# Performance work log

Measured on AMD Instinct MI355X. Metric: run time of the kernel, lower is better.

## Reference

```python
import jax, jax.numpy as jnp
import numpy as np

B, L, DIN = 2048, 70, 15
HID, NF, K = 16, 4, 40          # hidden_units//2, n_features, kernel_size
C = DIN + 1 + NF                # 20 signature input channels (original + time + conv features)
Z0 = 64
SIG_CH = C + C * C + C ** 3     # 8420, depth-3 signature channels


def setup_inputs() -> dict:
    key = jax.random.key(0)
    ks = jax.random.split(key, 8)
    return {
        "observed_data": jax.random.normal(ks[0], (B, L, DIN), jnp.float32),
        "observed_tp": jnp.linspace(0.0, 1.0, L, dtype=jnp.float32),
        "conv1_w": jax.random.normal(ks[1], (HID, DIN, K), jnp.float32) / np.float32(np.sqrt(DIN * K)),
        "conv1_b": jnp.zeros((HID,), jnp.float32),
        "conv2_w": jax.random.normal(ks[2], (HID, HID), jnp.float32) / np.float32(np.sqrt(HID)),
        "conv2_b": jnp.zeros((HID,), jnp.float32),
        "conv3_w": jax.random.normal(ks[3], (NF, HID), jnp.float32) / np.float32(np.sqrt(HID)),
        "conv3_b": jnp.zeros((NF,), jnp.float32),
        "w_out": jax.random.normal(ks[4], (2 * Z0, SIG_CH), jnp.float32) * np.float32(np.sqrt(2.0 / (SIG_CH + 2 * Z0))),
        "b_out": jnp.zeros((2 * Z0,), jnp.float32),
    }


def _augment(x, w1, b1, w2, b2, w3, b3):
    # x: (B, L, DIN).  signatory.Augment: conv(K) -> relu -> conv1x1 -> relu -> conv1x1,
    # then concat [truncated original, time channel, conv features] along channels.
    xc = jnp.transpose(x, (0, 2, 1))                                   # (B, DIN, L)
    h = jax.lax.conv_general_dilated(xc, w1, (1,), 'VALID')            # (B, HID, Lp)
    h = h + b1[None, :, None]
    h = jnp.einsum('oc,bcl->bol', w2, jax.nn.relu(h)) + b2[None, :, None]
    h = jnp.einsum('oc,bcl->bol', w3, jax.nn.relu(h)) + b3[None, :, None]
    conv_out = jnp.transpose(h, (0, 2, 1))                             # (B, Lp, NF)
    Lp = conv_out.shape[1]
    orig = x[:, K - 1:, :]                                             # (B, Lp, DIN)
    t = jnp.linspace(0.0, 1.0, Lp, dtype=x.dtype)
    time = jnp.broadcast_to(t[None, :, None], (x.shape[0], Lp, 1))
    return jnp.concatenate([orig, time, conv_out], axis=2)             # (B, Lp, C)


def _signature_depth3(path):
    # Truncated (depth 3) path signature with basepoint=True, via Chen's identity:
    # S <- S \otimes exp(dx) over increments, zero basepoint prepended.
    incs = jnp.diff(path, axis=1, prepend=jnp.zeros_like(path[:, :1]))  # (B, Lp, C)
    incs = jnp.transpose(incs, (1, 0, 2))                               # (Lp, B, C)
    Bn, Cn = path.shape[0], path.shape[2]
    s1 = jnp.zeros((Bn, Cn), path.dtype)
    s2 = jnp.zeros((Bn, Cn, Cn), path.dtype)
    s3 = jnp.zeros((Bn, Cn, Cn, Cn), path.dtype)

    def step(carry, d):
        s1, s2, s3 = carry
        e2 = 0.5 * d[:, :, None] * d[:, None, :]                        # d\otimes d / 2
        e3 = (e2[:, :, :, None] * d[:, None, None, :]) / 3.0            # d^{\otimes 3} / 6
        n3 = (s3
              + s2[:, :, :, None] * d[:, None, None, :]
              + s1[:, :, None, None] * e2[:, None, :, :]
              + e3)
        n2 = s2 + s1[:, :, None] * d[:, None, :] + e2
        n1 = s1 + d
        return (n1, n2, n3), None

    (s1, s2, s3), _ = jax.lax.scan(step, (s1, s2, s3), incs)
    return jnp.concatenate([s1, s2.reshape(Bn, -1), s3.reshape(Bn, -1)], axis=1)


def reference(observed_data, observed_tp, conv1_w, conv1_b, conv2_w, conv2_b,
              conv3_w, conv3_b, w_out, b_out):
    # encode_obs_time=False -> observed_tp unused
    path = _augment(observed_data, conv1_w, conv1_b, conv2_w, conv2_b, conv3_w, conv3_b)
    sig = _signature_depth3(path)                                       # (B, SIG_CH)
    z = sig @ w_out.T + b_out                                           # (B, 2*Z0)
    mean_z0 = z[:, :Z0][None]                                           # (1, B, Z0)
    std_z0 = jax.nn.softplus(z[:, Z0:][None])                           # (1, B, Z0)
    return mean_z0, std_z0
```

## Files before the change

kernel.cpp:

```cpp
#include <hip/hip_runtime.h>
#include <math.h>

#define B_TOT 2048
#define D_INC 15
#define KW    40
#define CCH   20
#define LP    31
#define SIGCH 8420
#define SIGP  8448
#define NOUT  128
#define KSPLIT 11
#define KLEN  768

typedef _Float16 f16;
typedef _Float16 f16x8 __attribute__((ext_vector_type(8)));
typedef _Float16 f16x4 __attribute__((ext_vector_type(4)));
typedef float    f32x4 __attribute__((ext_vector_type(4)));
typedef float    f32x2 __attribute__((ext_vector_type(2)));

__global__ __launch_bounds__(256) void k_prep(const float* __restrict__ w1,
                                              f16* __restrict__ wA)
{
    const int ln = threadIdx.x & 63;
    const int wv = threadIdx.x >> 6;
    const int h  = ln & 15;
    const int q4 = ln >> 4;
    for (int gi = 0; gi < 5; ++gi) {
        int g = wv * 5 + gi;
        f16x8 v;
#pragma unroll
        for (int j = 0; j < 8; ++j) {
            int kq = q4 * 8 + j;
            int kk = 2 * g + (kq >> 4);
            int c  = kq & 15;
            v[j] = (c < D_INC) ? (f16)w1[h * 600 + c * 40 + kk] : (f16)0.f;
        }
        *(f16x8*)(wA + g * 512 + ln * 8) = v;
    }
}

__global__ __launch_bounds__(256, 2) void k_augsig(
    const float* __restrict__ x,  const f16* __restrict__ wA, const float* __restrict__ b1,
    const float* __restrict__ w2, const float* __restrict__ b2,
    const float* __restrict__ w3, const float* __restrict__ b3,
    const float* __restrict__ w_out, f16* __restrict__ wh, f16* __restrict__ sig)
{
    if (blockIdx.x >= 512) {
        int t0 = (blockIdx.x - 512) * 256 + threadIdx.x;
        for (int chunk = t0; chunk < 128 * 1056; chunk += 8192) {
            int o  = chunk / 1056;
            int cw = chunk - o * 1056;
            int c0 = cw * 8;
            f16x8 v;
            if (c0 + 8 <= SIGCH) {
                const float* src = w_out + (size_t)o * SIGCH + c0;
                float4 a = *(const float4*)src;
                float4 b = *(const float4*)(src + 4);
                v = (f16x8){(f16)a.x,(f16)a.y,(f16)a.z,(f16)a.w,
                            (f16)b.x,(f16)b.y,(f16)b.z,(f16)b.w};
            } else {
#pragma unroll
                for (int e = 0; e < 8; ++e) {
                    int c = c0 + e;
                    v[e] = (c < SIGCH) ? (f16)w_out[(size_t)o * SIGCH + c] : (f16)0.f;
                }
            }
            *(f16x8*)(wh + (size_t)o * SIGP + c0) = v;
        }
        return;
    }

    __shared__ float xs[4 * 1068];
    __shared__ f16   xp16[4 * 1152];
    __shared__ float pprev[4 * 656];
    __shared__ float wsmall[356];
    float* w2s = wsmall;        float* b2s = wsmall + 256;
    float* w3s = wsmall + 272;  float* b3s = wsmall + 336;
    float* b1s = wsmall + 340;
    float* h1s  = (float*)xp16;
    float* incs = xs;

    const int tid = threadIdx.x;
    const int b0  = blockIdx.x * 4;

    for (int i = tid; i < 4 * 1050; i += 256) {
        int bl = i / 1050; int t = i - bl * 1050;
        xs[bl * 1068 + t] = x[(size_t)b0 * 1050 + i];
    }
    if (tid < 256) w2s[tid] = w2[tid];
    if (tid < 16)  b2s[tid] = b2[tid];
    if (tid < 64)  w3s[tid] = w3[tid];
    if (tid < 4)   b3s[tid] = b3[tid];
    if (tid < 16)  b1s[tid] = b1[tid];
    __syncthreads();

    for (int r = tid; r < 280; r += 256) {
        int bl = r / 70; int pos = r - bl * 70;
        const float* src = xs + bl * 1068 + pos * 15;
        f16* dst = xp16 + bl * 1152 + pos * 16;
#pragma unroll
        for (int c = 0; c < 15; ++c) dst[c] = (f16)src[c];
        dst[15] = (f16)0.f;
    }
    __syncthreads();

    const int lane = tid & 63;
    const int w    = tid >> 6;
    const int n16  = lane & 15;
    const int q4   = lane >> 4;

    f16x8 wa[20];
#pragma unroll
    for (int g = 0; g < 20; ++g) wa[g] = *(const f16x8*)(wA + g * 512 + lane * 8);

    f32x4 cacc[2];
#pragma unroll
    for (int tile = 0; tile < 2; ++tile) {
        const int pos0 = tile * 15;
        f32x4 acc = {0.f, 0.f, 0.f, 0.f};
#pragma unroll
        for (int g = 0; g < 20; ++g) {
            const f16x8 bf = *(const f16x8*)&xp16[w * 1152 +
                (pos0 + n16 + 2 * g + (q4 >> 1)) * 16 + (q4 & 1) * 8];
            acc = __builtin_amdgcn_mfma_f32_16x16x32_f16(wa[g], bf, acc, 0, 0, 0);
        }
        cacc[tile] = acc;
    }
    __syncthreads();

#pragma unroll
    for (int tile = 0; tile < 2; ++tile) {
        int pos = tile * 15 + n16;
#pragma unroll
        for (int r = 0; r < 4; ++r) {
            int h = q4 * 4 + r;
            h1s[(w * 31 + pos) * 17 + h] = fmaxf(cacc[tile][r] + b1s[h], 0.f);
        }
    }
    __syncthreads();

    if (tid < 124) {
        const int bl2 = tid / 31;
        const int pos = tid - bl2 * 31;
        float hr[16];
#pragma unroll
        for (int c2 = 0; c2 < 16; ++c2) hr[c2] = h1s[tid * 17 + c2];
        float h2[16];
#pragma unroll
        for (int o = 0; o < 16; ++o) {
            float s = b2s[o];
#pragma unroll
            for (int c2 = 0; c2 < 16; ++c2) s += w2s[o * 16 + c2] * hr[c2];
            h2[o] = fmaxf(s, 0.f);
        }
        float h3[4];
#pragma unroll
        for (int f = 0; f < 4; ++f) {
            float s = b3s[f];
#pragma unroll
            for (int c2 = 0; c2 < 16; ++c2) s += w3s[f * 16 + c2] * h2[c2];
            h3[f] = s;
        }
        float* pr = pprev + bl2 * 656 + 20 + pos * 20;
#pragma unroll
        for (int d = 0; d < D_INC; ++d) pr[d] = xs[bl2 * 1068 + (pos + 39) * 15 + d];
        pr[15] = (float)pos * (1.0f / 30.0f);
#pragma unroll
        for (int f = 0; f < 4; ++f) pr[16 + f] = h3[f];
    } else {
        int z = tid - 124;
        if (z < 80) pprev[(z / 20) * 656 + (z % 20)] = 0.f;
    }
    __syncthreads();

    float* pp = pprev + w * 656;
    float* ic = incs  + w * 624;
    for (int i = lane; i < 620; i += 64) ic[i] = pp[20 + i] - pp[i];
    __syncthreads();

    int iv[7], jv[7];
#pragma unroll
    for (int q = 0; q < 7; ++q) {
        int p = lane + 64 * q;
        iv[q] = p / 20; jv[q] = p - iv[q] * 20;
    }
    float s2r[7];
    f32x2 s3v[7][10];
#pragma unroll
    for (int q = 0; q < 7; ++q) {
        s2r[q] = 0.f;
#pragma unroll
        for (int k = 0; k < 10; ++k) s3v[q][k] = (f32x2){0.f, 0.f};
    }

    for (int t = 0; t < LP; ++t) {
        const float* ip = &ic[t * 20];
        const float* sp = &pp[t * 20];
        f32x2 dv[10];
        const float4* dp = (const float4*)ip;
#pragma unroll
        for (int r = 0; r < 5; ++r) {
            float4 v = dp[r];
            dv[2*r]   = (f32x2){v.x, v.y};
            dv[2*r+1] = (f32x2){v.z, v.w};
        }
#pragma unroll
        for (int q = 0; q < 7; ++q) {
            if (lane + 64 * q < 400) {
                const float di  = ip[iv[q]];
                const float dj  = ip[jv[q]];
                const float s1i = sp[iv[q]];
                const float t2  = s2r[q] + (0.5f * s1i + (1.0f / 6.0f) * di) * dj;
                const f32x2 t2v = {t2, t2};
#pragma unroll
                for (int k = 0; k < 10; ++k) s3v[q][k] += t2v * dv[k];
                s2r[q] += (s1i + 0.5f * di) * dj;
            }
        }
    }

    const int b = b0 + w;
    f16* sg = sig + (size_t)b * SIGP;
    if (lane < 20) sg[lane] = (f16)pp[620 + lane];
#pragma unroll
    for (int q = 0; q < 6; ++q) sg[20 + q * 64 + lane] = (f16)s2r[q];
    if (lane < 16) sg[404 + lane] = (f16)s2r[6];
#pragma unroll
    for (int q = 0; q < 7; ++q) {
        int p = lane + 64 * q;
        if (p < 400) {
            f16* base = sg + 420 + p * 20;
#pragma unroll
            for (int g = 0; g < 5; ++g) {
                f16x4 v = { (f16)s3v[q][2*g][0],   (f16)s3v[q][2*g][1],
                            (f16)s3v[q][2*g+1][0], (f16)s3v[q][2*g+1][1] };
                *(f16x4*)(base + 4 * g) = v;
            }
        }
    }
    if (lane < 28) sg[SIGCH + lane] = (f16)0.f;
}

__global__ __launch_bounds__(256) void k_gemm(const f16* __restrict__ sigh,
                                              const f16* __restrict__ wh,
                                              float* __restrict__ z_part)
{
    __shared__ f16 As[2048];
    __shared__ f16 Bs[8192];
    const int tid = threadIdx.x;
    const int l   = tid & 63;
    const int wv  = tid >> 6;
    const int mt  = blockIdx.x / KSPLIT;
    const int s   = blockIdx.x - mt * KSPLIT;
    const int m0  = mt * 32;
    const int kb  = s * KLEN;

    const f32x4 z4 = {0.f, 0.f, 0.f, 0.f};
    f32x4 acc[2][2];
    acc[0][0] = z4; acc[0][1] = z4; acc[1][0] = z4; acc[1][1] = z4;

    const size_t gA = (size_t)(m0 + (tid & 31)) * SIGP + kb + (tid >> 5) * 8;
    size_t gB[4];
#pragma unroll
    for (int r = 0; r < 4; ++r) {
        int slot = r * 256 + tid;
        gB[r] = (size_t)(slot & 127) * SIGP + kb + (slot >> 7) * 8;
    }

    f16x8 aR = *(const f16x8*)(sigh + gA);
    f16x8 bR[4];
#pragma unroll
    for (int r = 0; r < 4; ++r) bR[r] = *(const f16x8*)(wh + gB[r]);

    const int kg   = l >> 4;
    const int mrow = l & 15;

    for (int ch = 0; ch < 12; ++ch) {
        *(f16x8*)&As[tid * 8] = aR;
#pragma unroll
        for (int r = 0; r < 4; ++r) *(f16x8*)&Bs[(r * 256 + tid) * 8] = bR[r];
        __syncthreads();

        if (ch < 11) {
            int koff = (ch + 1) * 64;
            aR = *(const f16x8*)(sigh + gA + koff);
#pragma unroll
            for (int r = 0; r < 4; ++r) bR[r] = *(const f16x8*)(wh + gB[r] + koff);
        }

#pragma unroll
        for (int kc = 0; kc < 2; ++kc) {
            f16x8 aF[2], bF[2];
#pragma unroll
            for (int m2 = 0; m2 < 2; ++m2)
                aF[m2] = *(const f16x8*)&As[((kc * 4 + kg) * 32 + m2 * 16 + mrow) * 8];
#pragma unroll
            for (int n2 = 0; n2 < 2; ++n2)
                bF[n2] = *(const f16x8*)&Bs[((kc * 4 + kg) * 128 + wv * 32 + n2 * 16 + mrow) * 8];
#pragma unroll
            for (int m2 = 0; m2 < 2; ++m2)
#pragma unroll
                for (int n2 = 0; n2 < 2; ++n2)
                    acc[m2][n2] = __builtin_amdgcn_mfma_f32_16x16x32_f16(aF[m2], bF[n2], acc[m2][n2], 0, 0, 0);
        }
        __syncthreads();
    }

#pragma unroll
    for (int m2 = 0; m2 < 2; ++m2) {
#pragma unroll
        for (int n2 = 0; n2 < 2; ++n2) {
            int n = wv * 32 + n2 * 16 + (l & 15);
#pragma unroll
            for (int r = 0; r < 4; ++r) {
                int m = m0 + m2 * 16 + (l >> 4) * 4 + r;
                z_part[((size_t)s * B_TOT + m) * NOUT + n] = acc[m2][n2][r];
            }
        }
    }
}

__global__ __launch_bounds__(256) void k_final(const float* __restrict__ z_part,
                                               const float* __restrict__ b_out,
                                               float* __restrict__ out)
{
    int idx = blockIdx.x * 256 + threadIdx.x;
    int b = idx >> 7;
    int o = idx & 127;
    float z = b_out[o];
#pragma unroll
    for (int s = 0; s < KSPLIT; ++s) z += z_part[((size_t)s * B_TOT + b) * NOUT + o];
    if (o < 64) {
        out[(size_t)b * 64 + o] = z;
    } else {
        float sp = fmaxf(z, 0.f) + log1pf(expf(-fabsf(z)));
        out[131072 + (size_t)b * 64 + (o - 64)] = sp;
    }
}

extern "C" void kernel_launch(void* const* d_in, const int* in_sizes, int n_in,
                              void* d_out, int out_size, void* d_ws, size_t ws_size,
                              hipStream_t stream)
{
    const float* x     = (const float*)d_in[0];
    const float* w1    = (const float*)d_in[2];
    const float* b1    = (const float*)d_in[3];
    const float* w2    = (const float*)d_in[4];
    const float* b2    = (const float*)d_in[5];
    const float* w3    = (const float*)d_in[6];
    const float* b3    = (const float*)d_in[7];
    const float* w_out = (const float*)d_in[8];
    const float* b_out = (const float*)d_in[9];
    float* out = (float*)d_out;

    float* ws    = (float*)d_ws;
    f16*   sigh  = (f16*)ws;
    f16*   wh    = (f16*)(ws + 8650752);
    f16*   wA    = (f16*)(ws + 9191424);
    float* zpart = ws + 9196544;

    hipLaunchKernelGGL(k_prep,   dim3(1),    dim3(256), 0, stream, w1, wA);
    hipLaunchKernelGGL(k_augsig, dim3(544),  dim3(256), 0, stream,
                       x, wA, b1, w2, b2, w3, b3, w_out, wh, sigh);
    hipLaunchKernelGGL(k_gemm,   dim3(704),  dim3(256), 0, stream, sigh, wh, zpart);
    hipLaunchKernelGGL(k_final,  dim3(1024), dim3(256), 0, stream, zpart, b_out, out);
}
```

Measured before the change: 154.0 us.

## Compute depth-3 signature via MFMA over time with suffix-sum formulation

Replaces the per-lane sequential Chen-identity scan, which held 140 fp32 accumulators per lane, with a closed-form sum over time steps. Level-3 terms become products of per-step factors (a_i*d_j, e_i*d_j) contracted against a matrix of suffix sums of increments. Level 2 comes from a ones column. The contraction runs on 16x16x32 f16 MFMA. Shared memory is merged into one pool so per-warp buffers can reuse the input staging area. The change cuts register pressure and VALU work, at the cost of f16 rounding of the MFMA operands and extra shared-memory staging.

```diff
diff --git a/kernel.cpp b/kernel.cpp
--- a/kernel.cpp
+++ b/kernel.cpp
@@ -15,8 +15,8 @@
 typedef _Float16 f16;
 typedef _Float16 f16x8 __attribute__((ext_vector_type(8)));
 typedef _Float16 f16x4 __attribute__((ext_vector_type(4)));
+typedef _Float16 f16x2 __attribute__((ext_vector_type(2)));
 typedef float    f32x4 __attribute__((ext_vector_type(4)));
-typedef float    f32x2 __attribute__((ext_vector_type(2)));
 
 __global__ __launch_bounds__(256) void k_prep(const float* __restrict__ w1,
                                               f16* __restrict__ wA)
@@ -70,15 +70,15 @@
         return;
     }
 
-    __shared__ float xs[4 * 1068];
-    __shared__ f16   xp16[4 * 1152];
-    __shared__ float pprev[4 * 656];
-    __shared__ float wsmall[356];
+    __shared__ float pool[16228];
+    float* xs    = pool;
+    f16*   xp16  = (f16*)(pool + 4272);
+    float* h1s   = (float*)xp16;
+    float* pprev = pool + 13248;
+    float* wsmall= pool + 15872;
     float* w2s = wsmall;        float* b2s = wsmall + 256;
     float* w3s = wsmall + 272;  float* b3s = wsmall + 336;
     float* b1s = wsmall + 340;
-    float* h1s  = (float*)xp16;
-    float* incs = xs;
 
     const int tid = threadIdx.x;
     const int b0  = blockIdx.x * 4;
@@ -173,71 +173,92 @@
     }
     __syncthreads();
 
-    float* pp = pprev + w * 656;
-    float* ic = incs  + w * 624;
-    for (int i = lane; i < 620; i += 64) ic[i] = pp[20 + i] - pp[i];
-    __syncthreads();
-
-    int iv[7], jv[7];
-#pragma unroll
-    for (int q = 0; q < 7; ++q) {
-        int p = lane + 64 * q;
-        iv[q] = p / 20; jv[q] = p - iv[q] * 20;
-    }
-    float s2r[7];
-    f32x2 s3v[7][10];
-#pragma unroll
-    for (int q = 0; q < 7; ++q) {
-        s2r[q] = 0.f;
-#pragma unroll
-        for (int k = 0; k < 10; ++k) s3v[q][k] = (f32x2){0.f, 0.f};
-    }
-
-    for (int t = 0; t < LP; ++t) {
-        const float* ip = &ic[t * 20];
-        const float* sp = &pp[t * 20];
-        f32x2 dv[10];
-        const float4* dp = (const float4*)ip;
-#pragma unroll
-        for (int r = 0; r < 5; ++r) {
-            float4 v = dp[r];
-            dv[2*r]   = (f32x2){v.x, v.y};
-            dv[2*r+1] = (f32x2){v.z, v.w};
-        }
-#pragma unroll
-        for (int q = 0; q < 7; ++q) {
-            if (lane + 64 * q < 400) {
-                const float di  = ip[iv[q]];
-                const float dj  = ip[jv[q]];
-                const float s1i = sp[iv[q]];
-                const float t2  = s2r[q] + (0.5f * s1i + (1.0f / 6.0f) * di) * dj;
-                const f32x2 t2v = {t2, t2};
-#pragma unroll
-                for (int k = 0; k < 10; ++k) s3v[q][k] += t2v * dv[k];
-                s2r[q] += (s1i + 0.5f * di) * dj;
-            }
-        }
-    }
+    float* pp  = pprev + w * 656;
+    float* dtr = pool + w * 3312;
+    float* atr = dtr + 720;
+    float* etr = dtr + 1440;
+    f16*   Vb  = (f16*)(dtr + 2160);
+
+    for (int e = lane; e < 620; e += 64) {
+        int c = e / 31, t = e - c * 31;
+        float p0 = pp[t * 20 + c];
+        float d  = pp[(t + 1) * 20 + c] - p0;
+        dtr[c * 36 + t] = d;
+        atr[c * 36 + t] = p0 + 0.5f * d;
+        etr[c * 36 + t] = 0.5f * p0 + d * (1.0f / 6.0f);
+    }
+    if (lane < 20) {
+        dtr[lane * 36 + 31] = 0.f;
+        atr[lane * 36 + 31] = 0.f;
+        etr[lane * 36 + 31] = 0.f;
+    }
+    __syncthreads();
+
+    if (lane < 20) {
+        const int n = lane;
+        f16* vr = Vb + n * 72;
+        float s = 0.f;
+        for (int t = 30; t >= 0; --t) {
+            float dv = dtr[n * 36 + t];
+            vr[t]      = (f16)s;
+            vr[32 + t] = (f16)dv;
+            s += dv;
+        }
+        vr[31] = (f16)0.f;
+        vr[63] = (f16)0.f;
+    } else if (lane == 20) {
+        f16* vr = Vb + 20 * 72;
+        for (int k = 0; k < 64; ++k) vr[k] = (k < 31) ? (f16)1.f : (f16)0.f;
+    }
+    for (int e = lane; e < 11 * 32; e += 64) {
+        int row = 21 + (e >> 5);
+        int kk  = (e & 31) * 2;
+        *(f16x2*)(Vb + row * 72 + kk) = (f16x2){(f16)0.f, (f16)0.f};
+    }
+    __syncthreads();
+
+    f16x8 bf[2][2];
+#pragma unroll
+    for (int kc = 0; kc < 2; ++kc)
+#pragma unroll
+        for (int nt = 0; nt < 2; ++nt)
+            bf[kc][nt] = *(const f16x8*)(Vb + (nt * 16 + n16) * 72 + kc * 32 + q4 * 8);
 
     const int b = b0 + w;
     f16* sg = sig + (size_t)b * SIGP;
+
+    for (int mt = 0; mt < 25; ++mt) {
+        const int p = mt * 16 + n16;
+        const int i = p / 20, j = p - i * 20;
+        const float4* ap = (const float4*)(atr + i * 36 + q4 * 8);
+        const float4* ep = (const float4*)(etr + i * 36 + q4 * 8);
+        const float4* dp = (const float4*)(dtr + j * 36 + q4 * 8);
+        float4 a0 = ap[0], a1 = ap[1];
+        float4 e0 = ep[0], e1 = ep[1];
+        float4 d0 = dp[0], d1 = dp[1];
+        f16x8 uf, ef;
+        uf[0]=(f16)(a0.x*d0.x); uf[1]=(f16)(a0.y*d0.y); uf[2]=(f16)(a0.z*d0.z); uf[3]=(f16)(a0.w*d0.w);
+        uf[4]=(f16)(a1.x*d1.x); uf[5]=(f16)(a1.y*d1.y); uf[6]=(f16)(a1.z*d1.z); uf[7]=(f16)(a1.w*d1.w);
+        ef[0]=(f16)(e0.x*d0.x); ef[1]=(f16)(e0.y*d0.y); ef[2]=(f16)(e0.z*d0.z); ef[3]=(f16)(e0.w*d0.w);
+        ef[4]=(f16)(e1.x*d1.x); ef[5]=(f16)(e1.y*d1.y); ef[6]=(f16)(e1.z*d1.z); ef[7]=(f16)(e1.w*d1.w);
+
+        f32x4 acc0 = {0.f,0.f,0.f,0.f}, acc1 = {0.f,0.f,0.f,0.f};
+        acc0 = __builtin_amdgcn_mfma_f32_16x16x32_f16(uf, bf[0][0], acc0, 0, 0, 0);
+        acc0 = __builtin_amdgcn_mfma_f32_16x16x32_f16(ef, bf[1][0], acc0, 0, 0, 0);
+        acc1 = __builtin_amdgcn_mfma_f32_16x16x32_f16(uf, bf[0][1], acc1, 0, 0, 0);
+        acc1 = __builtin_amdgcn_mfma_f32_16x16x32_f16(ef, bf[1][1], acc1, 0, 0, 0);
+
+        const int prow0 = mt * 16 + q4 * 4;
+#pragma unroll
+        for (int r = 0; r < 4; ++r) {
+            const int p2 = prow0 + r;
+            sg[420 + p2 * 20 + n16] = (f16)acc0[r];
+            if (n16 < 4)       sg[420 + p2 * 20 + 16 + n16] = (f16)acc1[r];
+            else if (n16 == 4) sg[20 + p2] = (f16)acc1[r];
+        }
+    }
+
     if (lane < 20) sg[lane] = (f16)pp[620 + lane];
-#pragma unroll
-    for (int q = 0; q < 6; ++q) sg[20 + q * 64 + lane] = (f16)s2r[q];
-    if (lane < 16) sg[404 + lane] = (f16)s2r[6];
-#pragma unroll
-    for (int q = 0; q < 7; ++q) {
-        int p = lane + 64 * q;
-        if (p < 400) {
-            f16* base = sg + 420 + p * 20;
-#pragma unroll
-            for (int g = 0; g < 5; ++g) {
-                f16x4 v = { (f16)s3v[q][2*g][0],   (f16)s3v[q][2*g][1],
-                            (f16)s3v[q][2*g+1][0], (f16)s3v[q][2*g+1][1] };
-                *(f16x4*)(base + 4 * g) = v;
-            }
-        }
-    }
     if (lane < 28) sg[SIGCH + lane] = (f16)0.f;
 }
 
```

Measured after the change: 143.8 us. 6.6% less time.
